# Kernel tuning notes

Measured on AMD Instinct MI355X. Metric: run time of the kernel, lower is better.

The kernel has to match this reference:

```python
import jax, jax.numpy as jnp
import numpy as np

B, T, D = 2, 4096, 1024
H = 16
KD, VD = 512, 1024          # expand_k=0.5, expand_v=1.0
HK, HV = KD // H, VD // H   # 32, 64
CHUNK = 64
GATE_RANK = 16
GATE_NORM = 16.0            # gate_logit_normalizer
EPS = 1e-5


def setup_inputs() -> dict:
    key = jax.random.key(0)
    ks = jax.random.split(key, 10)
    w = lambda k, shape: (jax.random.normal(k, shape, jnp.float32) * 0.02)
    return {
        "x":      jax.random.normal(ks[0], (B, T, D), jnp.float32),
        "Wq":     w(ks[1], (D, KD)),
        "Wk":     w(ks[2], (D, KD)),
        "Wv":     w(ks[3], (D, VD)),
        "Wgk1":   w(ks[4], (D, GATE_RANK)),
        "Wgk2":   w(ks[5], (GATE_RANK, KD)),
        "bgk":    jnp.zeros((KD,), jnp.float32),
        "Wg":     w(ks[6], (D, VD)),
        "norm_w": jnp.ones((HV,), jnp.float32),
        "Wo":     w(ks[7], (VD, D)),
    }


def _split_chunks(t, hd):
    # [B, T, H*hd] -> [nC, B, H, C, hd]
    nC = T // CHUNK
    t = t.reshape(B, nC, CHUNK, H, hd)
    return jnp.transpose(t, (1, 0, 3, 2, 4))


def reference(x, Wq, Wk, Wv, Wgk1, Wgk2, bgk, Wg, norm_w, Wo):
    scale = HK ** -0.5
    q = _split_chunks(x @ Wq, HK)                       # [nC,B,H,C,HK]
    k = _split_chunks(x @ Wk, HK)
    v = _split_chunks(x @ Wv, HV)                       # [nC,B,H,C,HV]
    gk = jax.nn.log_sigmoid((x @ Wgk1) @ Wgk2 + bgk) / GATE_NORM
    gk = _split_chunks(gk, HK)                          # [nC,B,H,C,HK]

    mask = jnp.tril(jnp.ones((CHUNK, CHUNK), bool))

    def step(S, inp):
        qc, kc, vc, gc = inp                            # [B,H,C,hk/hv]
        b = jnp.cumsum(gc, axis=2)                      # cumulative log-decay
        qe = qc * jnp.exp(b) * scale
        # intra-chunk causal attention with relative decay exp(b_i - b_j)
        A = jnp.einsum('bhik,bhjk->bhij', qe, kc * jnp.exp(-b))
        A = jnp.where(mask, A, 0.0)
        o = jnp.einsum('bhij,bhjv->bhiv', A, vc)
        # inter-chunk contribution from carried state
        o = o + jnp.einsum('bhik,bhkv->bhiv', qe, S)
        b_last = b[:, :, -1]                            # [B,H,hk]
        ke = kc * jnp.exp(b_last[:, :, None, :] - b)
        S = jnp.exp(b_last)[..., None] * S + jnp.einsum('bhjk,bhjv->bhkv', ke, vc)
        return S, o

    S0 = jnp.zeros((B, H, HK, HV), x.dtype)
    _, o = jax.lax.scan(step, S0, (q, k, v, gk))        # o: [nC,B,H,C,HV]
    o = jnp.transpose(o, (1, 0, 3, 2, 4)).reshape(B, T, H, HV)

    # fused gated RMSNorm (FusedRMSNormSwishGate) per head
    g = (x @ Wg).reshape(B, T, H, HV)
    rms = o * jax.lax.rsqrt(jnp.mean(o * o, axis=-1, keepdims=True) + EPS) * norm_w
    out = rms * (g * jax.nn.sigmoid(g))
    return out.reshape(B, T, VD) @ Wo
```

## Files before the change

kernel.cpp:

```cpp
#include <hip/hip_runtime.h>
#include <cstddef>

#define B_   2
#define T_   4096
#define D_   1024
#define H_   16
#define KD_  512
#define VD_  1024
#define NC_  64
#define M_   (B_*T_)
#define GR_  16
#define EPS_ 1e-5f
#define SCALE_ 0.17677669529663687f
#define GNORM_INV_ (1.0f/16.0f)

#define NF_   3200
#define Q0_   0
#define K0_   512
#define V0_   1024
#define G0_   2048
#define GL0_  3072

typedef __attribute__((ext_vector_type(8))) __bf16 bf16x8;
typedef __attribute__((ext_vector_type(4))) float f32x4;

__device__ inline unsigned short f2bf(float f) {
  unsigned int u = __float_as_uint(f);
  u = (u + 0x7fffu + ((u >> 16) & 1u)) >> 16;
  return (unsigned short)u;
}
__device__ inline float bf2f(unsigned short u) {
  return __uint_as_float((unsigned int)u << 16);
}
__device__ inline void unpack8(uint4 u, float* f) {
  f[0] = bf2f(u.x & 0xffff); f[1] = bf2f(u.x >> 16);
  f[2] = bf2f(u.y & 0xffff); f[3] = bf2f(u.y >> 16);
  f[4] = bf2f(u.z & 0xffff); f[5] = bf2f(u.z >> 16);
  f[6] = bf2f(u.w & 0xffff); f[7] = bf2f(u.w >> 16);
}
__device__ inline uint4 pack8(const unsigned short* s) {
  uint4 u;
  u.x = (unsigned int)s[0] | ((unsigned int)s[1] << 16);
  u.y = (unsigned int)s[2] | ((unsigned int)s[3] << 16);
  u.z = (unsigned int)s[4] | ((unsigned int)s[5] << 16);
  u.w = (unsigned int)s[6] | ((unsigned int)s[7] << 16);
  return u;
}

__device__ __forceinline__ void gload_lds16(const unsigned short* g, unsigned short* l) {
  __builtin_amdgcn_global_load_lds(
      (const __attribute__((address_space(1))) unsigned int*)g,
      (__attribute__((address_space(3))) unsigned int*)l, 16, 0, 0);
}


__global__ __launch_bounds__(256) void k_prep(const float* __restrict__ x,
                                              const float* __restrict__ Wq,
                                              const float* __restrict__ Wk,
                                              const float* __restrict__ Wv,
                                              const float* __restrict__ Wg,
                                              const float* __restrict__ Wo,
                                              const float* __restrict__ Wgk1,
                                              unsigned short* __restrict__ xb,
                                              unsigned short* __restrict__ Wcat,
                                              unsigned short* __restrict__ woT) {
  __shared__ float tile[32][33];
  if (blockIdx.z >= 6) {
    int lin = ((blockIdx.z - 6) * 1024 + blockIdx.y * 32 + blockIdx.x) * 256 + threadIdx.x;
    int i = lin * 4;
    float4 f = *(const float4*)(x + i);
    ushort4 o;
    o.x = f2bf(f.x); o.y = f2bf(f.y); o.z = f2bf(f.z); o.w = f2bf(f.w);
    *(ushort4*)(xb + i) = o;
    return;
  }
  const float* in; unsigned short* out; int N;
  switch (blockIdx.z) {
    case 0: in = Wq;   out = Wcat + (size_t)Q0_ * D_;  N = 512;  break;
    case 1: in = Wk;   out = Wcat + (size_t)K0_ * D_;  N = 512;  break;
    case 2: in = Wv;   out = Wcat + (size_t)V0_ * D_;  N = 1024; break;
    case 3: in = Wg;   out = Wcat + (size_t)G0_ * D_;  N = 1024; break;
    case 4: in = Wo;   out = woT;                      N = 1024; break;
    default: in = Wgk1; out = Wcat + (size_t)GL0_ * D_; N = 128;  break;
  }
  int n0 = blockIdx.x * 32, k0 = blockIdx.y * 32;
  if (n0 >= N) return;
  int tx = threadIdx.x & 31, ty = threadIdx.x >> 5;
  if (blockIdx.z == 5) {
#pragma unroll
    for (int p = 0; p < 4; ++p)
      tile[ty + p*8][tx] = (n0 + tx < GR_) ? in[(size_t)(k0 + ty + p*8) * GR_ + n0 + tx] : 0.0f;
  } else {
#pragma unroll
    for (int p = 0; p < 4; ++p)
      tile[ty + p*8][tx] = in[(size_t)(k0 + ty + p*8) * N + n0 + tx];
  }
  __syncthreads();
#pragma unroll
  for (int p = 0; p < 4; ++p)
    out[(size_t)(n0 + ty + p*8) * 1024 + k0 + tx] = f2bf(tile[tx][ty + p*8]);
}


template <typename OutT>
__global__ __launch_bounds__(256, 3) void k_gemm_bt(const unsigned short* __restrict__ A,
                                                    const unsigned short* __restrict__ Bt,
                                                    OutT* __restrict__ C,
                                                    int M, int N, int K) {
  __shared__ __align__(16) unsigned short sA[128 * 64];
  __shared__ __align__(16) unsigned short sB[128 * 64];
  const int tid  = threadIdx.x;
  const int lane = tid & 63;
  const int wave = tid >> 6;
  const int wr = wave >> 1, wc = wave & 1;
  const int quad = lane >> 4, l16 = lane & 15;

  const int g = blockIdx.x;
  const int xcd = g & 7, slot = g >> 3;
  const int bm0 = ((xcd << 3) | (slot & 7)) << 7;
  const int bn0 = (slot >> 3) << 7;

  const int lrow = lane >> 3;
  const int gcol = ((lane & 7) ^ lrow) * 8;
  const unsigned short* ga = A  + (size_t)(bm0 + wave * 8 + lrow) * K + gcol;
  const unsigned short* gb = Bt + (size_t)(bn0 + wave * 8 + lrow) * K + gcol;
  unsigned short* la = sA + wave * 8 * 64;
  unsigned short* lb = sB + wave * 8 * 64;

  f32x4 acc[4][4] = {};

  for (int k0 = 0; k0 < K; k0 += 64) {
#pragma unroll
    for (int it = 0; it < 4; ++it) {
      gload_lds16(ga + k0 + (size_t)it * 32 * K, la + it * 32 * 64);
      gload_lds16(gb + k0 + (size_t)it * 32 * K, lb + it * 32 * 64);
    }
    __syncthreads();
#pragma unroll
    for (int kk = 0; kk < 2; ++kk) {
      bf16x8 af[4], bfv[4];
#pragma unroll
      for (int i = 0; i < 4; ++i) {
        int row = wr * 64 + i * 16 + l16;
        int gg = (kk * 4 + quad) ^ (row & 7);
        af[i] = *(const bf16x8*)(sA + row * 64 + gg * 8);
      }
#pragma unroll
      for (int j = 0; j < 4; ++j) {
        int row = wc * 64 + j * 16 + l16;
        int gg = (kk * 4 + quad) ^ (row & 7);
        bfv[j] = *(const bf16x8*)(sB + row * 64 + gg * 8);
      }
#pragma unroll
      for (int i = 0; i < 4; ++i)
#pragma unroll
        for (int j = 0; j < 4; ++j)
          acc[i][j] = __builtin_amdgcn_mfma_f32_16x16x32_bf16(af[i], bfv[j], acc[i][j], 0, 0, 0);
    }
    __syncthreads();
  }

#pragma unroll
  for (int i = 0; i < 4; ++i) {
    int row0 = bm0 + wr * 64 + i * 16 + quad * 4;
#pragma unroll
    for (int j = 0; j < 4; ++j) {
      int col = bn0 + wc * 64 + j * 16 + l16;
#pragma unroll
      for (int r = 0; r < 4; ++r) {
        float v = acc[i][j][r];
        if constexpr (sizeof(OutT) == 2)
          C[(size_t)(row0 + r) * N + col] = (OutT)f2bf(v);
        else
          C[(size_t)(row0 + r) * N + col] = (OutT)v;
      }
    }
  }
}


#define P1_SGLOW 0
#define P1_SW2   2048
#define P1_SBGK  4096
#define P1_VN    4224
#define P1_QEA   0
#define P1_KEB   5120
#define P1_KET   10240
#define P1_EBL   14848
#define P1_QN    14976
#define P1_KN    20096
#define P1_AL    P1_QN
#define P1_VT    25216
#define P1_SIZE  34432

__global__ __launch_bounds__(256, 4) void k_phase1(unsigned short* __restrict__ pbuf,
                                                   const float* __restrict__ Wgk2,
                                                   const float* __restrict__ bgk,
                                                   unsigned short* __restrict__ obuf,
                                                   unsigned short* __restrict__ Ut,
                                                   float* __restrict__ dvec) {
  const int bi = blockIdx.x;
  const int c = bi >> 5, bh = bi & 31;
  const int b = bh >> 4, h = bh & 15;
  const int tid = threadIdx.x;
  const int lane = tid & 63, w = tid >> 6;
  const int quad = lane >> 4, l16 = lane & 15;

  __shared__ __align__(16) char sm[P1_SIZE];

  const size_t row0 = (size_t)(b * T_ + c * 64);
  const size_t rq  = row0 * NF_ + Q0_ + h * 32;
  const size_t rk  = row0 * NF_ + K0_ + h * 32;
  const size_t rv  = row0 * NF_ + V0_ + h * 64;
  const size_t rgl = row0 * NF_ + GL0_;
  const size_t cb  = (size_t)c * 32 + bh;

  {
    int i = tid >> 2, seg = tid & 3;
    uint4 qu = *(const uint4*)(pbuf + rq + (size_t)i * NF_ + seg * 8);
    uint4 ku = *(const uint4*)(pbuf + rk + (size_t)i * NF_ + seg * 8);
    *(uint4*)(sm + P1_QN + i * 80 + seg * 16) = qu;
    *(uint4*)(sm + P1_KN + i * 80 + seg * 16) = ku;
  }
#pragma unroll
  for (int s = 0; s < 2; ++s) {
    int e = tid + s * 256;
    int j = e >> 3, seg = e & 7;
    uint4 vu = *(const uint4*)(pbuf + rv + (size_t)j * NF_ + seg * 8);
    *(uint4*)(sm + P1_VN + j * 144 + seg * 16) = vu;
  }
  if (tid < 128) {
    int i = tid >> 1, seg = tid & 1;
    uint4 gu = *(const uint4*)(pbuf + rgl + (size_t)i * NF_ + seg * 8);
    *(uint4*)(sm + P1_SGLOW + i * 32 + seg * 16) = gu;
    int r = tid >> 3, d4 = (tid & 7) * 4;
    *(float4*)(sm + P1_SW2 + (r * 32 + d4) * 4) = *(const float4*)(Wgk2 + r * KD_ + h * 32 + d4);
  }
  if (tid < 8)
    *(float4*)(sm + P1_SBGK + tid * 16) = *(const float4*)(bgk + h * 32 + tid * 4);
  __syncthreads();

  {
    int vd = tid & 63, jg = tid >> 6;
#pragma unroll
    for (int half = 0; half < 2; ++half) {
      int j0 = jg * 8 + half * 32;
      unsigned short t8[8];
#pragma unroll
      for (int jj = 0; jj < 8; ++jj)
        t8[jj] = *(const unsigned short*)(sm + P1_VN + (j0 + jj) * 144 + vd * 2);
      *(uint4*)(sm + P1_VT + vd * 144 + j0 * 2) = pack8(t8);
    }
  }

  {
    const int i = lane, dg = w;
    float gl[16];
    unpack8(*(const uint4*)(sm + P1_SGLOW + i * 32), gl);
    unpack8(*(const uint4*)(sm + P1_SGLOW + i * 32 + 16), gl + 8);
    float s[8];
    {
      float4 b0 = *(const float4*)(sm + P1_SBGK + dg * 32);
      float4 b1 = *(const float4*)(sm + P1_SBGK + dg * 32 + 16);
      s[0] = b0.x; s[1] = b0.y; s[2] = b0.z; s[3] = b0.w;
      s[4] = b1.x; s[5] = b1.y; s[6] = b1.z; s[7] = b1.w;
    }
#pragma unroll
    for (int r = 0; r < 16; ++r) {
      float4 wa = *(const float4*)(sm + P1_SW2 + (r * 32 + dg * 8) * 4);
      float4 wb = *(const float4*)(sm + P1_SW2 + (r * 32 + dg * 8) * 4 + 16);
      float gv = gl[r];
      s[0] += gv * wa.x; s[1] += gv * wa.y; s[2] += gv * wa.z; s[3] += gv * wa.w;
      s[4] += gv * wb.x; s[5] += gv * wb.y; s[6] += gv * wb.z; s[7] += gv * wb.w;
    }
    float bb[8];
#pragma unroll
    for (int j = 0; j < 8; ++j) {
      float ls = fminf(s[j], 0.0f) - __logf(1.0f + __expf(-fabsf(s[j])));
      float v = ls * GNORM_INV_;
#pragma unroll
      for (int off = 1; off < 64; off <<= 1) {
        int src = lane - off;
        float t2 = __shfl(v, src < 0 ? 0 : src, 64);
        if (lane >= off) v += t2;
      }
      bb[j] = v;
    }

    __syncthreads();

    if (lane == 63) {
      float ev[8];
#pragma unroll
      for (int j = 0; j < 8; ++j) {
        ev[j] = __expf(bb[j]);
        ((float*)(sm + P1_EBL))[dg * 8 + j] = ev[j];
      }
      float4 e0; e0.x = ev[0]; e0.y = ev[1]; e0.z = ev[2]; e0.w = ev[3];
      float4 e1; e1.x = ev[4]; e1.y = ev[5]; e1.z = ev[6]; e1.w = ev[7];
      *(float4*)(dvec + cb * 32 + dg * 8)     = e0;
      *(float4*)(dvec + cb * 32 + dg * 8 + 4) = e1;
    }
    float qf[8], kf[8];
    unpack8(*(const uint4*)(sm + P1_QN + i * 80 + dg * 16), qf);
    unpack8(*(const uint4*)(sm + P1_KN + i * 80 + dg * 16), kf);
    unsigned short qo[8], ko[8];
#pragma unroll
    for (int j = 0; j < 8; ++j) {
      float eb = __expf(bb[j]);
      float ie = __expf(-bb[j]);
      qo[j] = f2bf(qf[j] * eb * SCALE_);
      ko[j] = f2bf(kf[j] * ie);
      *(unsigned short*)(sm + P1_KET + (dg * 8 + j) * 144 + i * 2) = ko[j];
    }
    *(uint4*)(sm + P1_QEA + i * 80 + dg * 16) = pack8(qo);
    *(uint4*)(sm + P1_KEB + i * 80 + dg * 16) = pack8(ko);
  }
  __syncthreads();

  {
    int i = tid >> 2, seg = tid & 3;
    *(uint4*)(pbuf + rq + (size_t)i * NF_ + seg * 8) =
        *(const uint4*)(sm + P1_QEA + i * 80 + seg * 16);
  }

  const int tm = w;
  bf16x8 aq = *(const bf16x8*)(sm + P1_QEA + (tm * 16 + l16) * 80 + quad * 16);
  f32x4 cA[4] = {};
#pragma unroll
  for (int tn = 0; tn < 4; ++tn) {
    bf16x8 bk = *(const bf16x8*)(sm + P1_KEB + (tn * 16 + l16) * 80 + quad * 16);
    cA[tn] = __builtin_amdgcn_mfma_f32_16x16x32_bf16(aq, bk, cA[tn], 0, 0, 0);
  }

  {
    const int um = w >> 1;
    bf16x8 ak0 = *(const bf16x8*)(sm + P1_KET + (um * 16 + l16) * 144 + quad * 16);
    bf16x8 ak1 = *(const bf16x8*)(sm + P1_KET + (um * 16 + l16) * 144 + quad * 16 + 64);
    f32x4 cU[2] = {};
#pragma unroll
    for (int e = 0; e < 2; ++e) {
      int un = (w & 1) * 2 + e;
      bf16x8 bv0 = *(const bf16x8*)(sm + P1_VT + (un * 16 + l16) * 144 + quad * 16);
      bf16x8 bv1 = *(const bf16x8*)(sm + P1_VT + (un * 16 + l16) * 144 + quad * 16 + 64);
      cU[e] = __builtin_amdgcn_mfma_f32_16x16x32_bf16(ak0, bv0, cU[e], 0, 0, 0);
      cU[e] = __builtin_amdgcn_mfma_f32_16x16x32_bf16(ak1, bv1, cU[e], 0, 0, 0);
    }
    const int d0 = um * 16 + quad * 4;
    const float eb0 = ((const float*)(sm + P1_EBL))[d0];
    const float eb1 = ((const float*)(sm + P1_EBL))[d0 + 1];
    const float eb2 = ((const float*)(sm + P1_EBL))[d0 + 2];
    const float eb3 = ((const float*)(sm + P1_EBL))[d0 + 3];
#pragma unroll
    for (int e = 0; e < 2; ++e) {
      int un = (w & 1) * 2 + e;
      int vd = un * 16 + l16;
      unsigned long long u =
          (unsigned long long)((unsigned int)f2bf(cU[e][0] * eb0) |
                               ((unsigned int)f2bf(cU[e][1] * eb1) << 16)) |
          ((unsigned long long)((unsigned int)f2bf(cU[e][2] * eb2) |
                                ((unsigned int)f2bf(cU[e][3] * eb3) << 16)) << 32);
      *(unsigned long long*)(Ut + cb * 2048 + (size_t)vd * 32 + d0) = u;
    }
  }

#pragma unroll
  for (int tn = 0; tn < 4; ++tn)
#pragma unroll
    for (int r = 0; r < 4; ++r) {
      int row = tm * 16 + quad * 4 + r;
      int col = tn * 16 + l16;
      float av = (col <= row) ? cA[tn][r] : 0.0f;
      *(unsigned short*)(sm + P1_AL + row * 144 + col * 2) = f2bf(av);
    }
  __syncthreads();

  {
    bf16x8 aA0 = *(const bf16x8*)(sm + P1_AL + (tm * 16 + l16) * 144 + quad * 16);
    bf16x8 aA1 = *(const bf16x8*)(sm + P1_AL + (tm * 16 + l16) * 144 + quad * 16 + 64);
    unsigned short ob[16];
#pragma unroll
    for (int tn = 0; tn < 4; ++tn) {
      bf16x8 bv0 = *(const bf16x8*)(sm + P1_VT + (tn * 16 + l16) * 144 + quad * 16);
      bf16x8 bv1 = *(const bf16x8*)(sm + P1_VT + (tn * 16 + l16) * 144 + quad * 16 + 64);
      f32x4 co = {};
      co = __builtin_amdgcn_mfma_f32_16x16x32_bf16(aA0, bv0, co, 0, 0, 0);
      co = __builtin_amdgcn_mfma_f32_16x16x32_bf16(aA1, bv1, co, 0, 0, 0);
#pragma unroll
      for (int r = 0; r < 4; ++r)
        ob[tn * 4 + r] = f2bf(co[r]);
    }
    *(uint4*)(obuf + cb * 4096 + tid * 16)     = pack8(ob);
    *(uint4*)(obuf + cb * 4096 + tid * 16 + 8) = pack8(ob + 8);
  }
}


__global__ __launch_bounds__(128) void k_phase2(const unsigned short* __restrict__ Ut,
                                                const float* __restrict__ dvec,
                                                unsigned short* __restrict__ Sp) {
  int idx = blockIdx.x * 128 + threadIdx.x;
  int bh = idx >> 10, q = idx & 1023;
  int vd = q >> 4, d2 = (q & 15) * 2;
  float run0 = 0.0f, run1 = 0.0f;
  for (int c = 0; c < NC_; ++c) {
    size_t o = ((size_t)c * 32 + bh) * 2048 + vd * 32 + d2;
    unsigned int uu = *(const unsigned int*)(Ut + o);
    *(unsigned int*)(Sp + o) =
        (unsigned int)f2bf(run0) | ((unsigned int)f2bf(run1) << 16);
    float2 dv = *(const float2*)(dvec + ((size_t)c * 32 + bh) * 32 + d2);
    run0 = dv.x * run0 + bf2f(uu & 0xffff);
    run1 = dv.y * run1 + bf2f(uu >> 16);
  }
}


#define P3_QEA 0
#define P3_SL  5120
#define P3_OL  10240
#define P3_SIZE 27648

__global__ __launch_bounds__(256) void k_phase3rms(const unsigned short* __restrict__ pbuf,
                                                   const unsigned short* __restrict__ obuf,
                                                   const unsigned short* __restrict__ Sp,
                                                   const float* __restrict__ norm_w,
                                                   unsigned short* __restrict__ ybuf) {
  const int bi = blockIdx.x;
  const int c = bi >> 5, bh = bi & 31;
  const int b = bh >> 4, h = bh & 15;
  const int tid = threadIdx.x;
  const int lane = tid & 63, w = tid >> 6;
  const int quad = lane >> 4, l16 = lane & 15;

  __shared__ __align__(16) char sm[P3_SIZE];

  const size_t row0 = (size_t)(b * T_ + c * 64);
  const size_t rq = row0 * NF_ + Q0_ + h * 32;
  const size_t cb = (size_t)c * 32 + bh;

  {
    int i = tid >> 2, seg = tid & 3;
    *(uint4*)(sm + P3_QEA + i * 80 + seg * 16) =
        *(const uint4*)(pbuf + rq + (size_t)i * NF_ + seg * 8);
    *(uint4*)(sm + P3_SL + i * 80 + seg * 16) =
        *(const uint4*)(Sp + cb * 2048 + (size_t)i * 32 + seg * 8);
  }

  float obf[16];
  {
    uint4 o0 = *(const uint4*)(obuf + cb * 4096 + tid * 16);
    uint4 o1 = *(const uint4*)(obuf + cb * 4096 + tid * 16 + 8);
    unpack8(o0, obf);
    unpack8(o1, obf + 8);
  }
  __syncthreads();

  const int tm = w;
  bf16x8 aq = *(const bf16x8*)(sm + P3_QEA + (tm * 16 + l16) * 80 + quad * 16);
#pragma unroll
  for (int tn = 0; tn < 4; ++tn) {
    bf16x8 bs = *(const bf16x8*)(sm + P3_SL + (tn * 16 + l16) * 80 + quad * 16);
    f32x4 co = {};
    co = __builtin_amdgcn_mfma_f32_16x16x32_bf16(aq, bs, co, 0, 0, 0);
#pragma unroll
    for (int r = 0; r < 4; ++r) {
      int row = tm * 16 + quad * 4 + r;
      int col = tn * 16 + l16;
      float o = co[r] + obf[tn * 4 + r];
      *(float*)(sm + P3_OL + (row * 68 + col) * 4) = o;
    }
  }
  __syncthreads();

  {
    int r0 = tid >> 3, s8 = tid & 7;
#pragma unroll
    for (int half = 0; half < 2; ++half) {
      int row = r0 + half * 32;
      float4 a  = *(const float4*)(sm + P3_OL + (row * 68 + s8 * 8) * 4);
      float4 b4 = *(const float4*)(sm + P3_OL + (row * 68 + s8 * 8) * 4 + 16);
      float p = a.x*a.x + a.y*a.y + a.z*a.z + a.w*a.w
              + b4.x*b4.x + b4.y*b4.y + b4.z*b4.z + b4.w*b4.w;
      p += __shfl_xor(p, 1, 64);
      p += __shfl_xor(p, 2, 64);
      p += __shfl_xor(p, 4, 64);
      float rs = rsqrtf(p * (1.0f / 64.0f) + EPS_);
      size_t m = row0 + row;
      float gv[8];
      unpack8(*(const uint4*)(pbuf + m * NF_ + G0_ + h * 64 + s8 * 8), gv);
      float4 n0 = *(const float4*)(norm_w + s8 * 8);
      float4 n1 = *(const float4*)(norm_w + s8 * 8 + 4);
      float nw[8] = {n0.x, n0.y, n0.z, n0.w, n1.x, n1.y, n1.z, n1.w};
      float ov[8] = {a.x, a.y, a.z, a.w, b4.x, b4.y, b4.z, b4.w};
      unsigned short yo[8];
#pragma unroll
      for (int j = 0; j < 8; ++j) {
        float sw = gv[j] / (1.0f + __expf(-gv[j]));
        yo[j] = f2bf(ov[j] * rs * nw[j] * sw);
      }
      *(uint4*)(ybuf + m * VD_ + h * 64 + s8 * 8) = pack8(yo);
    }
  }
}


extern "C" void kernel_launch(void* const* d_in, const int* in_sizes, int n_in,
                              void* d_out, int out_size, void* d_ws, size_t ws_size,
                              hipStream_t stream) {
  const float* x    = (const float*)d_in[0];
  const float* Wq   = (const float*)d_in[1];
  const float* Wk   = (const float*)d_in[2];
  const float* Wv   = (const float*)d_in[3];
  const float* Wgk1 = (const float*)d_in[4];
  const float* Wgk2 = (const float*)d_in[5];
  const float* bgk  = (const float*)d_in[6];
  const float* Wg   = (const float*)d_in[7];
  const float* nw   = (const float*)d_in[8];
  const float* Wo   = (const float*)d_in[9];
  float* out = (float*)d_out;

  char* p = (char*)d_ws;
  unsigned short* xb   = (unsigned short*)p;  p += (size_t)M_ * D_ * 2;
  unsigned short* Wcat = (unsigned short*)p;  p += (size_t)NF_ * D_ * 2;
  unsigned short* woT  = (unsigned short*)p;  p += (size_t)D_ * VD_ * 2;
  unsigned short* pbuf = (unsigned short*)p;  p += (size_t)M_ * NF_ * 2;
  unsigned short* obuf = (unsigned short*)p;  p += (size_t)M_ * VD_ * 2;
  unsigned short* Ubuf = (unsigned short*)p;  p += (size_t)NC_ * 32 * 2048 * 2;
  unsigned short* Sbuf = (unsigned short*)p;  p += (size_t)NC_ * 32 * 2048 * 2;
  float* dbuf = (float*)p;                    p += (size_t)NC_ * 32 * 32 * 4;
  unsigned short* ybuf = (unsigned short*)p;  p += (size_t)M_ * VD_ * 2;

  k_prep<<<dim3(32, 32, 14), 256, 0, stream>>>(x, Wq, Wk, Wv, Wg, Wo, Wgk1, xb, Wcat, woT);

  k_gemm_bt<unsigned short><<<(NF_/128) * (M_/128), 256, 0, stream>>>(xb, Wcat, pbuf, M_, NF_, D_);

  k_phase1<<<NC_ * 32, 256, 0, stream>>>(pbuf, Wgk2, bgk, obuf, Ubuf, dbuf);
  k_phase2<<<256, 128, 0, stream>>>(Ubuf, dbuf, Sbuf);
  k_phase3rms<<<NC_ * 32, 256, 0, stream>>>(pbuf, obuf, Sbuf, nw, ybuf);

  k_gemm_bt<float><<<(D_/128) * (M_/128), 256, 0, stream>>>(ybuf, woT, out, M_, D_, VD_);
}
```

Baseline: 239.7 us.

## Replace fused projection GEMM with 256x256-tile double-buffered LDS kernel

Adds a new 256x256 tile GEMM with 512 threads that loads tiles directly from global memory into swizzled LDS, double-buffered, and uses an XCD-aware block swizzle with strip partitioning. It replaces the 128x128 GEMM for the fused input projection. The projection width is padded from 3200 to 3328 columns so it divides by 256, and the extra weight rows are zeroed with a memset. This adds wasted MFMA work on the padded columns and a larger pbuf row stride, which downstream kernels indexing pbuf by NF_ must tolerate.

```diff
diff --git a/kernel.cpp b/kernel.cpp
--- a/kernel.cpp
+++ b/kernel.cpp
@@ -14,7 +14,8 @@
 #define SCALE_ 0.17677669529663687f
 #define GNORM_INV_ (1.0f/16.0f)
 
-#define NF_   3200
+#define NF_   3328
+#define NVALID_ 3200
 #define Q0_   0
 #define K0_   512
 #define V0_   1024
@@ -179,6 +180,132 @@
 }
 
 
+#define SA_(BUF, COL)                                                              \
+  { char* d_ = smb + (BUF) * 65536 + stg;                                          \
+    gload_lds16(pa + (COL),                     (unsigned short*)(d_));            \
+    gload_lds16(pa + (COL) + (size_t)8 * Kv,    (unsigned short*)(d_ + 1024));     \
+    gload_lds16(pa + (COL) + (size_t)128 * Kv,  (unsigned short*)(d_ + 16384));    \
+    gload_lds16(pa + (COL) + (size_t)136 * Kv,  (unsigned short*)(d_ + 17408)); }
+
+#define SB_(BUF, COL)                                                              \
+  { char* d_ = smb + (BUF) * 65536 + 32768 + stg;                                  \
+    gload_lds16(pb + (COL),                     (unsigned short*)(d_));            \
+    gload_lds16(pb + (COL) + (size_t)8 * Kv,    (unsigned short*)(d_ + 1024));     \
+    gload_lds16(pb + (COL) + (size_t)128 * Kv,  (unsigned short*)(d_ + 16384));    \
+    gload_lds16(pb + (COL) + (size_t)136 * Kv,  (unsigned short*)(d_ + 17408)); }
+
+#define RD_A(QM, G0)                                                               \
+  _Pragma("unroll") for (int m_ = 0; m_ < 4; ++m_) {                               \
+    const int ra_ = (QM) * 64 + m_ * 16 + l16;                                     \
+    asm volatile("ds_read_b128 %0, %1" : "=v"(av[m_])                              \
+                 : "v"(lds3 + aRd + ra_ * 128 + (((G0) ^ (ra_ & 7)) * 16)));       \
+  }
+
+#define RD_B(G0)                                                                   \
+  _Pragma("unroll") for (int n_ = 0; n_ < 4; ++n_) {                               \
+    const int rn_ = (wc & 1) * 64 + n_ * 16 + l16;                                 \
+    asm volatile("ds_read_b128 %0, %1" : "=v"(bv[n_])                              \
+                 : "v"(lds3 + bRd + rn_ * 128 + (((G0) ^ (rn_ & 7)) * 16)));       \
+  }
+
+#define MFMA16(QM)                                                                 \
+  _Pragma("unroll") for (int n_ = 0; n_ < 4; ++n_)                                 \
+    _Pragma("unroll") for (int m_ = 0; m_ < 4; ++m_)                               \
+      acc[(QM)*4 + m_][n_] = __builtin_amdgcn_mfma_f32_16x16x32_bf16(              \
+          av[m_], bv[n_], acc[(QM)*4 + m_][n_], 0, 0, 0);
+
+#define PH_BODY(QM)                                                                \
+  __builtin_amdgcn_s_barrier();                                                    \
+  asm volatile("s_waitcnt lgkmcnt(0)" ::: "memory");                               \
+  __builtin_amdgcn_sched_barrier(0);                                               \
+  __builtin_amdgcn_s_setprio(1);                                                   \
+  MFMA16(QM)                                                                       \
+  __builtin_amdgcn_s_setprio(0);                                                   \
+  __builtin_amdgcn_s_barrier();
+
+#define TILE_(RB, STAGE_CODE, WAIT_CODE)                                           \
+  { const int aRd = (RB) * 65536 + wr * 16384;                                     \
+    const int bRd = (RB) * 65536 + 32768 + (wc >> 1) * 16384;                      \
+    RD_A(0, quad) RD_B(quad)                                                       \
+    PH_BODY(0)                                                                     \
+    RD_A(1, quad)                                                                  \
+    PH_BODY(1)                                                                     \
+    RD_A(0, 4 + quad) RD_B(4 + quad)                                               \
+    PH_BODY(0)                                                                     \
+    RD_A(1, 4 + quad)                                                              \
+    PH_BODY(1)                                                                     \
+    STAGE_CODE           \
+    WAIT_CODE                 \
+    __builtin_amdgcn_s_barrier(); }
+
+template <int Mv, int Nv, int Kv>
+__global__ __launch_bounds__(512, 2) void k_gemm256(const unsigned short* __restrict__ A,
+                                                    const unsigned short* __restrict__ Bt,
+                                                    unsigned short* __restrict__ C) {
+  constexpr int NT = Kv / 64;
+  constexpr int MTt = Mv / 256;
+  constexpr int NTt = Nv / 256;
+  constexpr int NWG = MTt * NTt;
+  constexpr int STRIP = 4;
+  static_assert(NWG % 8 == 0, "grid must be divisible by 8 for the XCD swizzle");
+  static_assert(MTt % STRIP == 0 && STRIP * NTt == NWG / 8,
+                "strip partition must give exactly one strip per XCD");
+  __shared__ __align__(16) char smb[131072];
+  const __attribute__((address_space(3))) char* lds3 =
+      (const __attribute__((address_space(3))) char*)smb;
+
+  const int tid  = threadIdx.x;
+  const int lane = tid & 63;
+  const int wv   = tid >> 6;
+  const int wr   = wv >> 2;
+  const int wc   = wv & 3;
+  const int quad = lane >> 4, l16 = lane & 15;
+
+  const int g   = blockIdx.x;
+  const int lin = (g & 7) * (NWG / 8) + (g >> 3);
+  const int bm0 = ((lin / (STRIP * NTt)) * STRIP + (lin & (STRIP - 1))) * 256;
+  const int bn0 = ((lin % (STRIP * NTt)) / STRIP) * 256;
+
+  const int srow = lane >> 3;
+  const int scol = ((lane & 7) ^ srow) * 8;
+  const unsigned short* pa = A  + (size_t)(bm0 + wv * 16 + srow) * Kv + scol;
+  const unsigned short* pb = Bt + (size_t)(bn0 + wv * 16 + srow) * Kv + scol;
+  const unsigned stg = (unsigned)(wv * 2048);
+
+  bf16x8 av[4], bv[4];
+  f32x4 acc[8][4] = {};
+
+  SA_(0, 0)  SB_(0, 0)
+  SA_(1, 64) SB_(1, 64)
+  asm volatile("s_waitcnt vmcnt(8)" ::: "memory");
+  __builtin_amdgcn_s_barrier();
+
+  size_t col = 128;
+#pragma unroll 2
+  for (int s = 0; s < NT - 2; ++s) {
+    const int rb = s & 1;
+    TILE_(rb,
+          SA_(rb, col) SB_(rb, col),
+          asm volatile("s_waitcnt vmcnt(8)" ::: "memory");)
+    col += 64;
+  }
+  TILE_(((NT - 2) & 1), , asm volatile("s_waitcnt vmcnt(0)" ::: "memory");)
+  TILE_(((NT - 1) & 1), , )
+
+#pragma unroll
+  for (int mi = 0; mi < 8; ++mi) {
+    const int row0 = bm0 + wr * 128 + mi * 16 + quad * 4;
+#pragma unroll
+    for (int n = 0; n < 4; ++n) {
+      const int col2 = bn0 + wc * 64 + n * 16 + l16;
+#pragma unroll
+      for (int r = 0; r < 4; ++r)
+        C[(size_t)(row0 + r) * Nv + col2] = f2bf(acc[mi][n][r]);
+    }
+  }
+}
+
+
 #define P1_SGLOW 0
 #define P1_SW2   2048
 #define P1_SBGK  4096
@@ -370,8 +497,8 @@
     for (int r = 0; r < 4; ++r) {
       int row = tm * 16 + quad * 4 + r;
       int col = tn * 16 + l16;
-      float av = (col <= row) ? cA[tn][r] : 0.0f;
-      *(unsigned short*)(sm + P1_AL + row * 144 + col * 2) = f2bf(av);
+      float av2 = (col <= row) ? cA[tn][r] : 0.0f;
+      *(unsigned short*)(sm + P1_AL + row * 144 + col * 2) = f2bf(av2);
     }
   __syncthreads();
 
@@ -530,9 +657,11 @@
   float* dbuf = (float*)p;                    p += (size_t)NC_ * 32 * 32 * 4;
   unsigned short* ybuf = (unsigned short*)p;  p += (size_t)M_ * VD_ * 2;
 
+  hipMemsetAsync(Wcat + (size_t)NVALID_ * D_, 0, (size_t)(NF_ - NVALID_) * D_ * 2, stream);
+
   k_prep<<<dim3(32, 32, 14), 256, 0, stream>>>(x, Wq, Wk, Wv, Wg, Wo, Wgk1, xb, Wcat, woT);
 
-  k_gemm_bt<unsigned short><<<(NF_/128) * (M_/128), 256, 0, stream>>>(xb, Wcat, pbuf, M_, NF_, D_);
+  k_gemm256<M_, NF_, D_><<<(M_ / 256) * (NF_ / 256), 512, 0, stream>>>(xb, Wcat, pbuf);
 
   k_phase1<<<NC_ * 32, 256, 0, stream>>>(pbuf, Wgk2, bgk, obuf, Ubuf, dbuf);
   k_phase2<<<256, 128, 0, stream>>>(Ubuf, dbuf, Sbuf);
```

After: 244.5 us. No clear change (+2.0%).
